# Kernel tuning notes

Measured on AMD Instinct MI355X. Metric: run time of the kernel, lower is better.

## Reference

```python
import jax, jax.numpy as jnp
import numpy as np

G = 16        # groups / heads
DG = 128      # per-group dim (2048/16)
F = 2048      # feat dim (representation_size)
N = 2048      # num_rois
M = 2048      # num_nongt_rois


def setup_inputs() -> dict:
    key = jax.random.key(0)
    ks = jax.random.split(key, 8)
    std = np.float32(0.02)
    return {
        "roi_feat": jax.random.normal(ks[0], (N, F), jnp.float32),
        "ref_feat": jax.random.normal(ks[1], (M, F), jnp.float32),
        "Wq_w": jax.random.normal(ks[2], (F, F), jnp.float32) * std,
        "Wq_b": jnp.zeros((F,), jnp.float32),
        "Wk_w": jax.random.normal(ks[3], (F, F), jnp.float32) * std,
        "Wk_b": jnp.zeros((F,), jnp.float32),
        # grouped 1x1 conv weight [2048, 2048, 1, 1] squeezed to [F, F];
        # group g maps input channels [g*F_g_in] -> output channels [g*DG:(g+1)*DG]
        "Wv_w": jax.random.normal(ks[4], (F, F), jnp.float32) * np.float32(0.01),
        "Wv_b": jnp.zeros((F,), jnp.float32),
    }


def reference(roi_feat, ref_feat, Wq_w, Wq_b, Wk_w, Wk_b, Wv_w, Wv_b):
    n = roi_feat.shape[0]
    scale = np.float32(1.0 / np.sqrt(DG))
    # torch Linear: y = x @ W.T + b
    q = (roi_feat @ Wq_w.T + Wq_b).reshape(n, G, DG)      # [N, G, DG]
    k = (ref_feat @ Wk_w.T + Wk_b).reshape(-1, G, DG)     # [M, G, DG]
    aff = jnp.einsum("ngd,mgd->ngm", q, k) * scale        # [N, G, M]
    attn = jax.nn.softmax(aff, axis=-1)
    # weighted values: v is raw ref_feat, per original
    ov = jnp.einsum("ngm,mf->ngf", attn, ref_feat)        # [N, G, F]
    # grouped 1x1 conv: per-group linear F -> DG
    Wv3 = Wv_w.reshape(G, DG, F)                          # [G, DG, F]
    out = jnp.einsum("ngf,gdf->ngd", ov, Wv3) + Wv_b.reshape(G, DG)
    return out.reshape(n, G * DG)                          # [N, F]
```

## Files before the change

kernel.cpp:

```cpp
#include <hip/hip_runtime.h>
#include <hip/hip_bf16.h>

#define G_   16
#define DG_  128
#define F_   2048
#define N_   2048
#define M_   2048

typedef __attribute__((ext_vector_type(8))) short s16x8;
typedef __attribute__((ext_vector_type(4))) float f32x4;
typedef __attribute__((ext_vector_type(2))) unsigned int u32x2;

typedef const __attribute__((address_space(1))) void GV;
typedef __attribute__((address_space(3))) void LV;

__device__ inline unsigned short f2bf(float f) {
  unsigned u = __float_as_uint(f);
  u += 0x7fffu + ((u >> 16) & 1u);
  return (unsigned short)(u >> 16);
}

struct Cvt5Args { const float* s[5]; unsigned short* d[5]; };

__global__ __launch_bounds__(256)
void cvt5(Cvt5Args a) {
  unsigned u = blockIdx.x * 256 + threadIdx.x;
  if (u >= 5u * 524288u) return;
  int seg = u >> 19;
  unsigned off = u & 524287u;
  const float4* sp = (const float4*)(a.s[seg] + (size_t)off * 8);
  float4 x = sp[0], y = sp[1];
  uint4 o;
  o.x = (unsigned)f2bf(x.x) | ((unsigned)f2bf(x.y) << 16);
  o.y = (unsigned)f2bf(x.z) | ((unsigned)f2bf(x.w) << 16);
  o.z = (unsigned)f2bf(y.x) | ((unsigned)f2bf(y.y) << 16);
  o.w = (unsigned)f2bf(y.z) | ((unsigned)f2bf(y.w) << 16);
  *(uint4*)(a.d[seg] + (size_t)off * 8) = o;
}

__global__ __launch_bounds__(256)
void cvt_bf16(const float* __restrict__ s, unsigned short* __restrict__ d, int n8) {
  int i = blockIdx.x * 256 + threadIdx.x;
  if (i >= n8) return;
  const float4* sp = (const float4*)(s + (size_t)i * 8);
  float4 a = sp[0], b = sp[1];
  uint4 o;
  o.x = (unsigned)f2bf(a.x) | ((unsigned)f2bf(a.y) << 16);
  o.y = (unsigned)f2bf(a.z) | ((unsigned)f2bf(a.w) << 16);
  o.z = (unsigned)f2bf(b.x) | ((unsigned)f2bf(b.y) << 16);
  o.w = (unsigned)f2bf(b.z) | ((unsigned)f2bf(b.w) << 16);
  *(uint4*)(d + (size_t)i * 8) = o;
}

struct GemmJobs {
  const unsigned short* A[3];
  const unsigned short* B[3];
  const float* bias[3];
  unsigned short* C[3];
  float osc[3];
};

__global__ __launch_bounds__(256, 2)
void gemm3(GemmJobs jb, int jbase) {
  __shared__ unsigned short As[2][128 * 64];
  __shared__ unsigned short Bs[2][128 * 64];
  const int j = jbase + (blockIdx.x >> 8);
  const int bs = blockIdx.x & 255;
  const unsigned short* A = jb.A[j];
  const unsigned short* B = jb.B[j];
  const float* bias = jb.bias[j];
  unsigned short* C = jb.C[j];
  const float osc = jb.osc[j];

  const int tid = threadIdx.x, lane = tid & 63, wv = tid >> 6;
  const int wm = wv >> 1, wn = wv & 1;
  const int l15 = lane & 15, l4 = lane >> 4;
  const int m0 = (bs >> 4) * 128, n0 = (bs & 15) * 128;

  f32x4 acc[4][4];
#pragma unroll
  for (int i = 0; i < 4; ++i)
#pragma unroll
    for (int jj = 0; jj < 4; ++jj) acc[i][jj] = (f32x4){0.f, 0.f, 0.f, 0.f};

  const int ksw = (((lane & 7) ^ (lane >> 3)) * 8);
  const size_t baseA = (size_t)(m0 + wv * 32 + (lane >> 3)) * F_ + ksw;
  const size_t baseB = (size_t)(n0 + wv * 32 + (lane >> 3)) * F_ + ksw;

  auto stage = [&](int buf, int k0) {
#pragma unroll
    for (int i = 0; i < 4; ++i) {
      __builtin_amdgcn_global_load_lds((GV*)(A + baseA + (size_t)i * 8 * F_ + k0),
                                       (LV*)(&As[buf][(wv * 32 + i * 8) * 64]), 16, 0, 0);
      __builtin_amdgcn_global_load_lds((GV*)(B + baseB + (size_t)i * 8 * F_ + k0),
                                       (LV*)(&Bs[buf][(wv * 32 + i * 8) * 64]), 16, 0, 0);
    }
  };

  stage(0, 0);
  __syncthreads();
  int cur = 0;
  const int xorb = (l15 & 7) << 4;
  const int csw0 = (l4 * 16) ^ xorb;
  const int csw1 = (64 + l4 * 16) ^ xorb;

  const int NT = F_ / 64;
  for (int t = 0; t < NT; ++t) {
    if (t + 1 < NT) stage(cur ^ 1, (t + 1) * 64);
    const unsigned short* Ab = &As[cur][0];
    const unsigned short* Bb = &Bs[cur][0];
#pragma unroll
    for (int kc = 0; kc < 2; ++kc) {
      const int cs = kc ? csw1 : csw0;
      s16x8 af[4], bf[4];
#pragma unroll
      for (int i = 0; i < 4; ++i)
        af[i] = *(const s16x8*)((const char*)Ab + (wm * 64 + i * 16 + l15) * 128 + cs);
#pragma unroll
      for (int i = 0; i < 4; ++i)
        bf[i] = *(const s16x8*)((const char*)Bb + (wn * 64 + i * 16 + l15) * 128 + cs);
      __builtin_amdgcn_s_setprio(1);
#pragma unroll
      for (int am = 0; am < 4; ++am)
#pragma unroll
        for (int bn = 0; bn < 4; ++bn)
          acc[am][bn] = __builtin_amdgcn_mfma_f32_16x16x32_bf16(af[am], bf[bn], acc[am][bn], 0, 0, 0);
      __builtin_amdgcn_s_setprio(0);
    }
    __syncthreads();
    cur ^= 1;
  }

#pragma unroll
  for (int bn = 0; bn < 4; ++bn) {
    int c = n0 + wn * 64 + bn * 16 + l15;
    float bv = bias ? bias[c] : 0.f;
#pragma unroll
    for (int am = 0; am < 4; ++am) {
#pragma unroll
      for (int jj = 0; jj < 4; ++jj) {
        int r = m0 + wm * 64 + am * 16 + l4 * 4 + jj;
        C[(size_t)r * F_ + c] = f2bf((acc[am][bn][jj] + bv) * osc);
      }
    }
  }
}

__global__ __launch_bounds__(256, 2)
void attn_mfma(const unsigned short* __restrict__ Q,
               const unsigned short* __restrict__ K,
               const unsigned short* __restrict__ Vt,
               const float* __restrict__ vb,
               float* __restrict__ out) {
  __shared__ unsigned short Kt[2][64 * 128];
  __shared__ unsigned short Vts[2][128 * 64];
  __shared__ unsigned short Pt[4][16 * 64];
  const int tid = threadIdx.x, lane = tid & 63, wv = tid >> 6;
  const int l15 = lane & 15, l4 = lane >> 4;
  const int g = blockIdx.y;
  const int q0 = blockIdx.x * 64 + wv * 16;

  s16x8 qa[4];
#pragma unroll
  for (int kc = 0; kc < 4; ++kc)
    qa[kc] = *(const s16x8*)(Q + (size_t)(q0 + l15) * F_ + g * DG_ + kc * 32 + l4 * 8);

  f32x4 oa[8];
#pragma unroll
  for (int df = 0; df < 8; ++df) oa[df] = (f32x4){0.f, 0.f, 0.f, 0.f};
  float m_r = -1e30f, l_r = 0.f;

  const int ksw0 = (((lane & 15) ^ (lane >> 4)) * 8);
  const int ksw1 = (((lane & 15) ^ 4 ^ (lane >> 4)) * 8);
  const int vsw  = (((lane & 7) ^ (lane >> 3)) * 8);
  const int xorb = (l15 & 7) << 4;
  int csw[4];
#pragma unroll
  for (int kc = 0; kc < 4; ++kc) csw[kc] = (kc * 64 + l4 * 16) ^ xorb;

  auto stage = [&](int buf, int kv0) {
#pragma unroll
    for (int i = 0; i < 4; ++i) {
      int r0 = wv * 16 + i * 4;
      __builtin_amdgcn_global_load_lds(
          (GV*)(K + (size_t)(kv0 + r0 + (lane >> 4)) * F_ + g * DG_ + ((i & 1) ? ksw1 : ksw0)),
          (LV*)(&Kt[buf][r0 * 128]), 16, 0, 0);
    }
#pragma unroll
    for (int i = 0; i < 4; ++i) {
      int r0 = wv * 32 + i * 8;
      __builtin_amdgcn_global_load_lds(
          (GV*)(Vt + (size_t)(g * DG_ + r0 + (lane >> 3)) * M_ + kv0 + vsw),
          (LV*)(&Vts[buf][r0 * 64]), 16, 0, 0);
    }
  };

  stage(0, 0);
  __syncthreads();
  int cur = 0;
  unsigned short* Pw = &Pt[wv][0];

  for (int t = 0; t < M_ / 64; ++t) {
    if (t + 1 < M_ / 64) stage(cur ^ 1, (t + 1) * 64);
    const unsigned short* Kb = &Kt[cur][0];
    const unsigned short* Vb = &Vts[cur][0];

    f32x4 sf[4];
    __builtin_amdgcn_s_setprio(1);
#pragma unroll
    for (int kvf = 0; kvf < 4; ++kvf) {
      f32x4 s = (f32x4){0.f, 0.f, 0.f, 0.f};
#pragma unroll
      for (int kc = 0; kc < 4; ++kc) {
        s16x8 kf = *(const s16x8*)((const char*)Kb + (kvf * 16 + l15) * 256 + csw[kc]);
        s = __builtin_amdgcn_mfma_f32_16x16x32_bf16(kf, qa[kc], s, 0, 0, 0);
      }
      sf[kvf] = s;
    }
    __builtin_amdgcn_s_setprio(0);

    float tmax = sf[0][0];
#pragma unroll
    for (int kvf = 0; kvf < 4; ++kvf) {
      tmax = fmaxf(tmax, fmaxf(fmaxf(sf[kvf][0], sf[kvf][1]),
                               fmaxf(sf[kvf][2], sf[kvf][3])));
    }
    tmax = fmaxf(tmax, __shfl_xor(tmax, 16));
    tmax = fmaxf(tmax, __shfl_xor(tmax, 32));
    if (!__all(tmax <= m_r + 8.0f)) {
      float mnew = fmaxf(m_r, tmax);
      float corr = __builtin_amdgcn_exp2f(m_r - mnew);
      m_r = mnew;
      l_r *= corr;
      float c0 = __shfl(corr, l4 * 4 + 0);
      float c1 = __shfl(corr, l4 * 4 + 1);
      float c2 = __shfl(corr, l4 * 4 + 2);
      float c3 = __shfl(corr, l4 * 4 + 3);
#pragma unroll
      for (int df = 0; df < 8; ++df) {
        oa[df][0] *= c0; oa[df][1] *= c1; oa[df][2] *= c2; oa[df][3] *= c3;
      }
    }

    float psum = 0.f;
#pragma unroll
    for (int kvf = 0; kvf < 4; ++kvf) {
      float p0 = __builtin_amdgcn_exp2f(sf[kvf][0] - m_r);
      float p1 = __builtin_amdgcn_exp2f(sf[kvf][1] - m_r);
      float p2 = __builtin_amdgcn_exp2f(sf[kvf][2] - m_r);
      float p3 = __builtin_amdgcn_exp2f(sf[kvf][3] - m_r);
      psum += (p0 + p1) + (p2 + p3);
      u32x2 w;
      asm("v_cvt_pk_bf16_f32 %0, %1, %2" : "=v"(w.x) : "v"(p0), "v"(p1));
      asm("v_cvt_pk_bf16_f32 %0, %1, %2" : "=v"(w.y) : "v"(p2), "v"(p3));
      *(u32x2*)((char*)Pw + l15 * 128 + ((kvf * 32 + l4 * 8) ^ xorb)) = w;
    }
    psum += __shfl_xor(psum, 16);
    psum += __shfl_xor(psum, 32);
    l_r += psum;

    s16x8 pa0 = *(const s16x8*)((const char*)Pw + l15 * 128 + csw[0]);
    s16x8 pa1 = *(const s16x8*)((const char*)Pw + l15 * 128 + csw[1]);
    __builtin_amdgcn_s_setprio(1);
#pragma unroll
    for (int df = 0; df < 8; ++df) {
      s16x8 v0 = *(const s16x8*)((const char*)Vb + (df * 16 + l15) * 128 + csw[0]);
      s16x8 v1 = *(const s16x8*)((const char*)Vb + (df * 16 + l15) * 128 + csw[1]);
      oa[df] = __builtin_amdgcn_mfma_f32_16x16x32_bf16(pa0, v0, oa[df], 0, 0, 0);
      oa[df] = __builtin_amdgcn_mfma_f32_16x16x32_bf16(pa1, v1, oa[df], 0, 0, 0);
    }
    __builtin_amdgcn_s_setprio(0);
    __syncthreads();
    cur ^= 1;
  }

  float linv = 1.0f / l_r;
  float i0 = __shfl(linv, l4 * 4 + 0);
  float i1 = __shfl(linv, l4 * 4 + 1);
  float i2 = __shfl(linv, l4 * 4 + 2);
  float i3 = __shfl(linv, l4 * 4 + 3);
#pragma unroll
  for (int df = 0; df < 8; ++df) {
    int c = g * DG_ + df * 16 + l15;
    float bv = vb[c];
    out[(size_t)(q0 + l4 * 4 + 0) * F_ + c] = oa[df][0] * i0 + bv;
    out[(size_t)(q0 + l4 * 4 + 1) * F_ + c] = oa[df][1] * i1 + bv;
    out[(size_t)(q0 + l4 * 4 + 2) * F_ + c] = oa[df][2] * i2 + bv;
    out[(size_t)(q0 + l4 * 4 + 3) * F_ + c] = oa[df][3] * i3 + bv;
  }
}

extern "C" void kernel_launch(void* const* d_in, const int* in_sizes, int n_in,
                              void* d_out, int out_size, void* d_ws, size_t ws_size,
                              hipStream_t stream) {
  const float* roi  = (const float*)d_in[0];
  const float* ref  = (const float*)d_in[1];
  const float* Wq_w = (const float*)d_in[2];
  const float* Wq_b = (const float*)d_in[3];
  const float* Wk_w = (const float*)d_in[4];
  const float* Wk_b = (const float*)d_in[5];
  const float* Wv_w = (const float*)d_in[6];
  const float* Wv_b = (const float*)d_in[7];
  float* out = (float*)d_out;
  const size_t SEG = 4194304;
  const float cscale = 0.12751664508246770f;

  if (ws_size >= 64ull * 1024 * 1024) {
    unsigned short* roi_bf = (unsigned short*)d_ws;
    unsigned short* ref_bf = roi_bf + SEG;
    unsigned short* Wq_bf  = ref_bf + SEG;
    unsigned short* Wk_bf  = Wq_bf + SEG;
    unsigned short* Wv_bf  = Wk_bf + SEG;
    unsigned short* Qb     = Wv_bf + SEG;
    unsigned short* Kb     = Qb + SEG;
    unsigned short* Vtb    = Kb + SEG;

    Cvt5Args ca;
    ca.s[0] = roi;  ca.d[0] = roi_bf;
    ca.s[1] = ref;  ca.d[1] = ref_bf;
    ca.s[2] = Wq_w; ca.d[2] = Wq_bf;
    ca.s[3] = Wk_w; ca.d[3] = Wk_bf;
    ca.s[4] = Wv_w; ca.d[4] = Wv_bf;
    cvt5<<<10240, 256, 0, stream>>>(ca);

    GemmJobs jb;
    jb.A[0] = roi_bf; jb.B[0] = Wq_bf;  jb.bias[0] = Wq_b;    jb.C[0] = Qb;  jb.osc[0] = cscale;
    jb.A[1] = ref_bf; jb.B[1] = Wk_bf;  jb.bias[1] = Wk_b;    jb.C[1] = Kb;  jb.osc[1] = 1.0f;
    jb.A[2] = Wv_bf;  jb.B[2] = ref_bf; jb.bias[2] = nullptr; jb.C[2] = Vtb; jb.osc[2] = 1.0f;
    gemm3<<<768, 256, 0, stream>>>(jb, 0);

    attn_mfma<<<dim3(N_ / 64, G_), 256, 0, stream>>>(Qb, Kb, Vtb, Wv_b, out);
  } else {
    if (ws_size < 48ull * 1024 * 1024) return;
    unsigned short* roi_bf = (unsigned short*)d_ws;
    unsigned short* ref_bf = roi_bf + SEG;
    unsigned short* W_bf   = ref_bf + SEG;
    unsigned short* Qb     = W_bf + SEG;
    unsigned short* Kb     = Qb + SEG;
    unsigned short* Vtb    = Kb + SEG;
    const int n8 = (N_ * F_) / 8;

    cvt_bf16<<<2048, 256, 0, stream>>>(roi, roi_bf, n8);
    cvt_bf16<<<2048, 256, 0, stream>>>(ref, ref_bf, n8);

    GemmJobs jb;
    jb.A[0] = roi_bf; jb.B[0] = W_bf;   jb.bias[0] = Wq_b;    jb.C[0] = Qb;  jb.osc[0] = cscale;
    jb.A[1] = ref_bf; jb.B[1] = W_bf;   jb.bias[1] = Wk_b;    jb.C[1] = Kb;  jb.osc[1] = 1.0f;
    jb.A[2] = W_bf;   jb.B[2] = ref_bf; jb.bias[2] = nullptr; jb.C[2] = Vtb; jb.osc[2] = 1.0f;

    cvt_bf16<<<2048, 256, 0, stream>>>(Wq_w, W_bf, n8);
    gemm3<<<256, 256, 0, stream>>>(jb, 0);
    cvt_bf16<<<2048, 256, 0, stream>>>(Wk_w, W_bf, n8);
    gemm3<<<256, 256, 0, stream>>>(jb, 1);
    cvt_bf16<<<2048, 256, 0, stream>>>(Wv_w, W_bf, n8);
    gemm3<<<256, 256, 0, stream>>>(jb, 2);

    attn_mfma<<<dim3(N_ / 64, G_), 256, 0, stream>>>(Qb, Kb, Vtb, Wv_b, out);
  }
}
```

Before: 150.3 us.

## Use 256x256-tile 8-wave GEMM with interleaved prefetch for projections

Replaces the 128x128-tile, 4-wave projection GEMM with a 256x256-tile, 512-thread kernel using 128 KB of LDS. Prefetch of the next k-tile is split into quarter loads interleaved with four MFMA phases, each separated by explicit barriers and waitcnts. The larger tile is meant to raise arithmetic intensity and cut global and LDS traffic per FLOP. In exchange the grid drops to 192 blocks (fewer than the CU count), register pressure rises, and more barriers are added. The fallback path for smaller workspaces is removed.

```diff
diff --git a/kernel.cpp b/kernel.cpp
--- a/kernel.cpp
+++ b/kernel.cpp
@@ -38,20 +38,6 @@
   *(uint4*)(a.d[seg] + (size_t)off * 8) = o;
 }
 
-__global__ __launch_bounds__(256)
-void cvt_bf16(const float* __restrict__ s, unsigned short* __restrict__ d, int n8) {
-  int i = blockIdx.x * 256 + threadIdx.x;
-  if (i >= n8) return;
-  const float4* sp = (const float4*)(s + (size_t)i * 8);
-  float4 a = sp[0], b = sp[1];
-  uint4 o;
-  o.x = (unsigned)f2bf(a.x) | ((unsigned)f2bf(a.y) << 16);
-  o.y = (unsigned)f2bf(a.z) | ((unsigned)f2bf(a.w) << 16);
-  o.z = (unsigned)f2bf(b.x) | ((unsigned)f2bf(b.y) << 16);
-  o.w = (unsigned)f2bf(b.z) | ((unsigned)f2bf(b.w) << 16);
-  *(uint4*)(d + (size_t)i * 8) = o;
-}
-
 struct GemmJobs {
   const unsigned short* A[3];
   const unsigned short* B[3];
@@ -60,12 +46,11 @@
   float osc[3];
 };
 
-__global__ __launch_bounds__(256, 2)
-void gemm3(GemmJobs jb, int jbase) {
-  __shared__ unsigned short As[2][128 * 64];
-  __shared__ unsigned short Bs[2][128 * 64];
-  const int j = jbase + (blockIdx.x >> 8);
-  const int bs = blockIdx.x & 255;
+__global__ __launch_bounds__(512, 2)
+void gemm8(GemmJobs jb) {
+  __shared__ __align__(16) char lds[131072];
+  const int j  = blockIdx.x >> 6;
+  const int bs = blockIdx.x & 63;
   const unsigned short* A = jb.A[j];
   const unsigned short* B = jb.B[j];
   const float* bias = jb.bias[j];
@@ -73,74 +58,139 @@
   const float osc = jb.osc[j];
 
   const int tid = threadIdx.x, lane = tid & 63, wv = tid >> 6;
-  const int wm = wv >> 1, wn = wv & 1;
+  const int wm = wv >> 2, wn = wv & 3;
   const int l15 = lane & 15, l4 = lane >> 4;
-  const int m0 = (bs >> 4) * 128, n0 = (bs & 15) * 128;
-
-  f32x4 acc[4][4];
-#pragma unroll
-  for (int i = 0; i < 4; ++i)
-#pragma unroll
-    for (int jj = 0; jj < 4; ++jj) acc[i][jj] = (f32x4){0.f, 0.f, 0.f, 0.f};
-
-  const int ksw = (((lane & 7) ^ (lane >> 3)) * 8);
-  const size_t baseA = (size_t)(m0 + wv * 32 + (lane >> 3)) * F_ + ksw;
-  const size_t baseB = (size_t)(n0 + wv * 32 + (lane >> 3)) * F_ + ksw;
-
-  auto stage = [&](int buf, int k0) {
-#pragma unroll
-    for (int i = 0; i < 4; ++i) {
-      __builtin_amdgcn_global_load_lds((GV*)(A + baseA + (size_t)i * 8 * F_ + k0),
-                                       (LV*)(&As[buf][(wv * 32 + i * 8) * 64]), 16, 0, 0);
-      __builtin_amdgcn_global_load_lds((GV*)(B + baseB + (size_t)i * 8 * F_ + k0),
-                                       (LV*)(&Bs[buf][(wv * 32 + i * 8) * 64]), 16, 0, 0);
+  const int m0 = (bs >> 3) * 256, n0 = (bs & 7) * 256;
+  const int xo  = (l15 & 7) << 4;
+  const int ksw = ((lane & 7) ^ (lane >> 3)) * 8;
+  const int brr0 = (wn & 1) * 64;
+
+  f32x4 acc[8][4];
+#pragma unroll
+  for (int i = 0; i < 8; ++i)
+#pragma unroll
+    for (int nf = 0; nf < 4; ++nf) acc[i][nf] = (f32x4){0.f, 0.f, 0.f, 0.f};
+
+  auto stage_half = [&](int buf2, const unsigned short* Mat, int lbase,
+                        int h, int row0, int k0) {
+#pragma unroll
+    for (int c = 0; c < 2; ++c) {
+      __builtin_amdgcn_global_load_lds(
+          (GV*)(Mat + (size_t)(row0 + h * 128 + c * 64 + wv * 8 + (lane >> 3)) * F_
+                + k0 + ksw),
+          (LV*)(lds + buf2 * 65536 + lbase + h * 16384 + c * 8192 + wv * 1024),
+          16, 0, 0);
     }
   };
 
-  stage(0, 0);
-  __syncthreads();
-  int cur = 0;
-  const int xorb = (l15 & 7) << 4;
-  const int csw0 = (l4 * 16) ^ xorb;
-  const int csw1 = (64 + l4 * 16) ^ xorb;
+  stage_half(0, A, 0,     0, m0, 0);
+  stage_half(0, A, 0,     1, m0, 0);
+  stage_half(0, B, 32768, 0, n0, 0);
+  stage_half(0, B, 32768, 1, n0, 0);
+  asm volatile("s_waitcnt vmcnt(0)" ::: "memory");
+  __builtin_amdgcn_sched_barrier(0);
+  __builtin_amdgcn_s_barrier();
 
   const int NT = F_ / 64;
   for (int t = 0; t < NT; ++t) {
-    if (t + 1 < NT) stage(cur ^ 1, (t + 1) * 64);
-    const unsigned short* Ab = &As[cur][0];
-    const unsigned short* Bb = &Bs[cur][0];
-#pragma unroll
-    for (int kc = 0; kc < 2; ++kc) {
-      const int cs = kc ? csw1 : csw0;
-      s16x8 af[4], bf[4];
-#pragma unroll
-      for (int i = 0; i < 4; ++i)
-        af[i] = *(const s16x8*)((const char*)Ab + (wm * 64 + i * 16 + l15) * 128 + cs);
-#pragma unroll
-      for (int i = 0; i < 4; ++i)
-        bf[i] = *(const s16x8*)((const char*)Bb + (wn * 64 + i * 16 + l15) * 128 + cs);
-      __builtin_amdgcn_s_setprio(1);
-#pragma unroll
-      for (int am = 0; am < 4; ++am)
-#pragma unroll
-        for (int bn = 0; bn < 4; ++bn)
-          acc[am][bn] = __builtin_amdgcn_mfma_f32_16x16x32_bf16(af[am], bf[bn], acc[am][bn], 0, 0, 0);
-      __builtin_amdgcn_s_setprio(0);
-    }
-    __syncthreads();
-    cur ^= 1;
+    const int buf = t & 1;
+    const char* Ab = lds + buf * 65536 + wm * 16384;
+    const char* Bb = lds + buf * 65536 + 32768 + (wn >> 1) * 16384;
+    const bool pf = (t + 1 < NT);
+    const int k1 = (t + 1) * 64;
+    s16x8 af[4], bf[4];
+
+    auto ldA = [&](int mf, int ks) {
+      return *(const s16x8*)(Ab + (mf * 16 + l15) * 128 + ((ks * 64 + l4 * 16) ^ xo));
+    };
+    auto ldB = [&](int nf, int ks) {
+      return *(const s16x8*)(Bb + (brr0 + nf * 16 + l15) * 128 + ((ks * 64 + l4 * 16) ^ xo));
+    };
+
+#pragma unroll
+    for (int nf = 0; nf < 4; ++nf) bf[nf] = ldB(nf, 0);
+#pragma unroll
+    for (int i = 0; i < 4; ++i) af[i] = ldA(i, 0);
+    if (pf) stage_half(buf ^ 1, A, 0, 0, m0, k1);
+    __builtin_amdgcn_sched_barrier(0);
+    __builtin_amdgcn_s_barrier();
+    asm volatile("s_waitcnt lgkmcnt(0)" ::: "memory");
+    __builtin_amdgcn_sched_barrier(0);
+    __builtin_amdgcn_s_setprio(1);
+#pragma unroll
+    for (int i = 0; i < 4; ++i)
+#pragma unroll
+      for (int nf = 0; nf < 4; ++nf)
+        acc[i][nf] = __builtin_amdgcn_mfma_f32_16x16x32_bf16(af[i], bf[nf], acc[i][nf], 0, 0, 0);
+    __builtin_amdgcn_s_setprio(0);
+    __builtin_amdgcn_sched_barrier(0);
+    __builtin_amdgcn_s_barrier();
+
+#pragma unroll
+    for (int i = 0; i < 4; ++i) af[i] = ldA(4 + i, 0);
+    if (pf) stage_half(buf ^ 1, A, 0, 1, m0, k1);
+    __builtin_amdgcn_sched_barrier(0);
+    __builtin_amdgcn_s_barrier();
+    asm volatile("s_waitcnt lgkmcnt(0)" ::: "memory");
+    __builtin_amdgcn_sched_barrier(0);
+    __builtin_amdgcn_s_setprio(1);
+#pragma unroll
+    for (int i = 0; i < 4; ++i)
+#pragma unroll
+      for (int nf = 0; nf < 4; ++nf)
+        acc[4 + i][nf] = __builtin_amdgcn_mfma_f32_16x16x32_bf16(af[i], bf[nf], acc[4 + i][nf], 0, 0, 0);
+    __builtin_amdgcn_s_setprio(0);
+    __builtin_amdgcn_sched_barrier(0);
+    __builtin_amdgcn_s_barrier();
+
+#pragma unroll
+    for (int nf = 0; nf < 4; ++nf) bf[nf] = ldB(nf, 1);
+#pragma unroll
+    for (int i = 0; i < 4; ++i) af[i] = ldA(i, 1);
+    if (pf) stage_half(buf ^ 1, B, 32768, 0, n0, k1);
+    __builtin_amdgcn_sched_barrier(0);
+    __builtin_amdgcn_s_barrier();
+    asm volatile("s_waitcnt lgkmcnt(0)" ::: "memory");
+    __builtin_amdgcn_sched_barrier(0);
+    __builtin_amdgcn_s_setprio(1);
+#pragma unroll
+    for (int i = 0; i < 4; ++i)
+#pragma unroll
+      for (int nf = 0; nf < 4; ++nf)
+        acc[i][nf] = __builtin_amdgcn_mfma_f32_16x16x32_bf16(af[i], bf[nf], acc[i][nf], 0, 0, 0);
+    __builtin_amdgcn_s_setprio(0);
+    __builtin_amdgcn_sched_barrier(0);
+    __builtin_amdgcn_s_barrier();
+
+#pragma unroll
+    for (int i = 0; i < 4; ++i) af[i] = ldA(4 + i, 1);
+    if (pf) stage_half(buf ^ 1, B, 32768, 1, n0, k1);
+    __builtin_amdgcn_sched_barrier(0);
+    __builtin_amdgcn_s_barrier();
+    asm volatile("s_waitcnt lgkmcnt(0)" ::: "memory");
+    __builtin_amdgcn_sched_barrier(0);
+    __builtin_amdgcn_s_setprio(1);
+#pragma unroll
+    for (int i = 0; i < 4; ++i)
+#pragma unroll
+      for (int nf = 0; nf < 4; ++nf)
+        acc[4 + i][nf] = __builtin_amdgcn_mfma_f32_16x16x32_bf16(af[i], bf[nf], acc[4 + i][nf], 0, 0, 0);
+    __builtin_amdgcn_s_setprio(0);
+    asm volatile("s_waitcnt vmcnt(0)" ::: "memory");
+    __builtin_amdgcn_sched_barrier(0);
+    __builtin_amdgcn_s_barrier();
   }
 
 #pragma unroll
-  for (int bn = 0; bn < 4; ++bn) {
-    int c = n0 + wn * 64 + bn * 16 + l15;
+  for (int nf = 0; nf < 4; ++nf) {
+    int c = n0 + wn * 64 + nf * 16 + l15;
     float bv = bias ? bias[c] : 0.f;
 #pragma unroll
-    for (int am = 0; am < 4; ++am) {
+    for (int mf = 0; mf < 8; ++mf) {
 #pragma unroll
       for (int jj = 0; jj < 4; ++jj) {
-        int r = m0 + wm * 64 + am * 16 + l4 * 4 + jj;
-        C[(size_t)r * F_ + c] = f2bf((acc[am][bn][jj] + bv) * osc);
+        int r = m0 + wm * 128 + mf * 16 + l4 * 4 + jj;
+        C[(size_t)r * F_ + c] = f2bf((acc[mf][nf][jj] + bv) * osc);
       }
     }
   }
@@ -305,56 +355,29 @@
   const size_t SEG = 4194304;
   const float cscale = 0.12751664508246770f;
 
-  if (ws_size >= 64ull * 1024 * 1024) {
-    unsigned short* roi_bf = (unsigned short*)d_ws;
-    unsigned short* ref_bf = roi_bf + SEG;
-    unsigned short* Wq_bf  = ref_bf + SEG;
-    unsigned short* Wk_bf  = Wq_bf + SEG;
-    unsigned short* Wv_bf  = Wk_bf + SEG;
-    unsigned short* Qb     = Wv_bf + SEG;
-    unsigned short* Kb     = Qb + SEG;
-    unsigned short* Vtb    = Kb + SEG;
-
-    Cvt5Args ca;
-    ca.s[0] = roi;  ca.d[0] = roi_bf;
-    ca.s[1] = ref;  ca.d[1] = ref_bf;
-    ca.s[2] = Wq_w; ca.d[2] = Wq_bf;
-    ca.s[3] = Wk_w; ca.d[3] = Wk_bf;
-    ca.s[4] = Wv_w; ca.d[4] = Wv_bf;
-    cvt5<<<10240, 256, 0, stream>>>(ca);
-
-    GemmJobs jb;
-    jb.A[0] = roi_bf; jb.B[0] = Wq_bf;  jb.bias[0] = Wq_b;    jb.C[0] = Qb;  jb.osc[0] = cscale;
-    jb.A[1] = ref_bf; jb.B[1] = Wk_bf;  jb.bias[1] = Wk_b;    jb.C[1] = Kb;  jb.osc[1] = 1.0f;
-    jb.A[2] = Wv_bf;  jb.B[2] = ref_bf; jb.bias[2] = nullptr; jb.C[2] = Vtb; jb.osc[2] = 1.0f;
-    gemm3<<<768, 256, 0, stream>>>(jb, 0);
-
-    attn_mfma<<<dim3(N_ / 64, G_), 256, 0, stream>>>(Qb, Kb, Vtb, Wv_b, out);
-  } else {
-    if (ws_size < 48ull * 1024 * 1024) return;
-    unsigned short* roi_bf = (unsigned short*)d_ws;
-    unsigned short* ref_bf = roi_bf + SEG;
-    unsigned short* W_bf   = ref_bf + SEG;
-    unsigned short* Qb     = W_bf + SEG;
-    unsigned short* Kb     = Qb + SEG;
-    unsigned short* Vtb    = Kb + SEG;
-    const int n8 = (N_ * F_) / 8;
-
-    cvt_bf16<<<2048, 256, 0, stream>>>(roi, roi_bf, n8);
-    cvt_bf16<<<2048, 256, 0, stream>>>(ref, ref_bf, n8);
-
-    GemmJobs jb;
-    jb.A[0] = roi_bf; jb.B[0] = W_bf;   jb.bias[0] = Wq_b;    jb.C[0] = Qb;  jb.osc[0] = cscale;
-    jb.A[1] = ref_bf; jb.B[1] = W_bf;   jb.bias[1] = Wk_b;    jb.C[1] = Kb;  jb.osc[1] = 1.0f;
-    jb.A[2] = W_bf;   jb.B[2] = ref_bf; jb.bias[2] = nullptr; jb.C[2] = Vtb; jb.osc[2] = 1.0f;
-
-    cvt_bf16<<<2048, 256, 0, stream>>>(Wq_w, W_bf, n8);
-    gemm3<<<256, 256, 0, stream>>>(jb, 0);
-    cvt_bf16<<<2048, 256, 0, stream>>>(Wk_w, W_bf, n8);
-    gemm3<<<256, 256, 0, stream>>>(jb, 1);
-    cvt_bf16<<<2048, 256, 0, stream>>>(Wv_w, W_bf, n8);
-    gemm3<<<256, 256, 0, stream>>>(jb, 2);
-
-    attn_mfma<<<dim3(N_ / 64, G_), 256, 0, stream>>>(Qb, Kb, Vtb, Wv_b, out);
-  }
-}
+  if (ws_size < 64ull * 1024 * 1024) return;
+  unsigned short* roi_bf = (unsigned short*)d_ws;
+  unsigned short* ref_bf = roi_bf + SEG;
+  unsigned short* Wq_bf  = ref_bf + SEG;
+  unsigned short* Wk_bf  = Wq_bf + SEG;
+  unsigned short* Wv_bf  = Wk_bf + SEG;
+  unsigned short* Qb     = Wv_bf + SEG;
+  unsigned short* Kb     = Qb + SEG;
+  unsigned short* Vtb    = Kb + SEG;
+
+  Cvt5Args ca;
+  ca.s[0] = roi;  ca.d[0] = roi_bf;
+  ca.s[1] = ref;  ca.d[1] = ref_bf;
+  ca.s[2] = Wq_w; ca.d[2] = Wq_bf;
+  ca.s[3] = Wk_w; ca.d[3] = Wk_bf;
+  ca.s[4] = Wv_w; ca.d[4] = Wv_bf;
+  cvt5<<<10240, 256, 0, stream>>>(ca);
+
+  GemmJobs jb;
+  jb.A[0] = roi_bf; jb.B[0] = Wq_bf;  jb.bias[0] = Wq_b;    jb.C[0] = Qb;  jb.osc[0] = cscale;
+  jb.A[1] = ref_bf; jb.B[1] = Wk_bf;  jb.bias[1] = Wk_b;    jb.C[1] = Kb;  jb.osc[1] = 1.0f;
+  jb.A[2] = Wv_bf;  jb.B[2] = ref_bf; jb.bias[2] = nullptr; jb.C[2] = Vtb; jb.osc[2] = 1.0f;
+  gemm8<<<192, 512, 0, stream>>>(jb);
+
+  attn_mfma<<<dim3(N_ / 64, G_), 256, 0, stream>>>(Qb, Kb, Vtb, Wv_b, out);
+}
```

After: 141.6 us. 5.8% less time.
